# Kernel optimization log

Measured on AMD Instinct MI355X. Metric: run time of the kernel, lower is better.

## Reference

```python
import jax, jax.numpy as jnp
import numpy as np

B, T, C, H = 4, 2048, 1024, 16
D = C // H  # head dim = 64

def setup_inputs() -> dict:
    key = jax.random.key(0)
    ks = jax.random.split(key, 9)
    s = 1.0 / np.sqrt(C)
    return {
        "x":  jax.random.normal(ks[0], (B, T, C), jnp.float32),
        "Wq": jax.random.normal(ks[1], (C, C), jnp.float32) * s,
        "bq": jax.random.normal(ks[2], (C,), jnp.float32) * 0.02,
        "Wk": jax.random.normal(ks[3], (C, C), jnp.float32) * s,
        "bk": jax.random.normal(ks[4], (C,), jnp.float32) * 0.02,
        "Wv": jax.random.normal(ks[5], (C, C), jnp.float32) * s,
        "bv": jax.random.normal(ks[6], (C,), jnp.float32) * 0.02,
        "Wp": jax.random.normal(ks[7], (C, C), jnp.float32) * s,
        "bp": jax.random.normal(ks[8], (C,), jnp.float32) * 0.02,
    }

def reference(x, Wq, bq, Wk, bk, Wv, bv, Wp, bp):
    Bx, Tx, Cx = x.shape
    # projections; PyTorch Linear computes x @ W.T + b
    q = (x @ Wq.T + bq).reshape(Bx, Tx, H, D).transpose(0, 2, 1, 3)  # [B,H,T,D]
    k = (x @ Wk.T + bk).reshape(Bx, Tx, H, D).transpose(0, 2, 1, 3)
    v = (x @ Wv.T + bv).reshape(Bx, Tx, H, D).transpose(0, 2, 1, 3)
    att = jnp.einsum('bhtd,bhsd->bhts', q, k) * (1.0 / np.sqrt(D))  # [B,H,T,T]
    causal = jnp.tril(jnp.ones((Tx, Tx), bool))
    att = jnp.where(causal[None, None], att, -jnp.inf)
    att = jax.nn.softmax(att, axis=-1)
    y = jnp.einsum('bhts,bhsd->bhtd', att, v)  # [B,H,T,D]
    y = y.transpose(0, 2, 1, 3).reshape(Bx, Tx, Cx)
    return y @ Wp.T + bp
```

## Files before the change

kernel.cpp:

```cpp
#include <hip/hip_runtime.h>
#include <hip/hip_bf16.h>
#include <math.h>

static constexpr int Bn = 4, Tlen = 2048, Cdim = 1024, Hn = 16, Dh = 64;
static constexpr int Mtot = Bn * Tlen;

typedef __attribute__((ext_vector_type(8)))  short    s16x8;
typedef __attribute__((ext_vector_type(4)))  float    f32x4;
typedef __attribute__((ext_vector_type(16))) float    f32x16;
typedef __attribute__((ext_vector_type(2)))  unsigned u32x2;
typedef unsigned short u16;

#define QSCALE 0.18033688011112042f

__device__ __forceinline__ u16 f2bf(float f) {
    union { float f; unsigned u; } x; x.f = f;
    unsigned r = x.u + 0x7FFFu + ((x.u >> 16) & 1u);
    return (u16)(r >> 16);
}
__device__ __forceinline__ unsigned cvtpk(float lo, float hi) {
    unsigned r;
    asm("v_cvt_pk_bf16_f32 %0, %1, %2" : "=v"(r) : "v"(lo), "v"(hi));
    return r;
}
__device__ __forceinline__ void lane32swap(unsigned& a, unsigned& b) {
    asm("v_permlane32_swap_b32 %0, %1" : "+v"(a), "+v"(b));
}
__device__ __forceinline__ void gload_lds16(const void* g, void* l) {
    __builtin_amdgcn_global_load_lds(
        (const __attribute__((address_space(1))) void*)g,
        (__attribute__((address_space(3))) void*)l, 16, 0, 0);
}

__global__ __launch_bounds__(256) void cvt_bf16(const float* __restrict__ in,
                                                u16* __restrict__ out) {
    size_t i = (size_t)(blockIdx.x * 256 + threadIdx.x) * 8;
    float4 a = *(const float4*)(in + i);
    float4 b = *(const float4*)(in + i + 4);
    s16x8 o;
    o[0] = (short)f2bf(a.x); o[1] = (short)f2bf(a.y);
    o[2] = (short)f2bf(a.z); o[3] = (short)f2bf(a.w);
    o[4] = (short)f2bf(b.x); o[5] = (short)f2bf(b.y);
    o[6] = (short)f2bf(b.z); o[7] = (short)f2bf(b.w);
    *(s16x8*)(out + i) = o;
}

template <int MODE, int NB>
__global__ __launch_bounds__(512, 4) void gemm8w(const u16* __restrict__ A,
                                                 const u16* __restrict__ Bm,
                                                 const float* __restrict__ bq,
                                                 const float* __restrict__ bk,
                                                 const float* __restrict__ bv,
                                                 void* __restrict__ out0,
                                                 u16* __restrict__ vt) {
    constexpr int K = Cdim;
    constexpr int NKT = K / 32;
    __shared__ u16 As[3][128 * 32];
    __shared__ u16 Bs[3][256 * 32];

    const int f  = blockIdx.x;
    const int f2 = (f & 7) * (8 * NB) + (f >> 3);
    const int bm = f2 / NB, bn = f2 % NB;
    const int m0 = bm * 128, n0g = bn * 256;

    const int tid = threadIdx.x, lane = tid & 63, w = tid >> 6;
    const int wm = w >> 2, wn = w & 3;
    const int rowA = lane & 15, kg = lane >> 4;

    const int srow  = w * 16 + (lane >> 2);
    const int scolA = (((lane & 3) ^ (srow & 3)) * 8);
    const u16* Ab  = A  + (size_t)(m0 + srow) * K + scolA;
    const u16* Bb0 = Bm + (size_t)(n0g + srow) * K + scolA;
    const u16* Bb1 = Bm + (size_t)(n0g + 128 + srow) * K + scolA;

#define STAGE_T(KT, BUF)                                              \
    do {                                                              \
        const int k0_ = (KT) * 32;                                    \
        gload_lds16(Ab  + k0_, &As[BUF][w * 512]);                    \
        gload_lds16(Bb0 + k0_, &Bs[BUF][w * 512]);                    \
        gload_lds16(Bb1 + k0_, &Bs[BUF][4096 + w * 512]);             \
    } while (0)

    const int fswz = ((kg ^ (rowA & 3)) * 8);
    const int aoff = (wm * 64 + rowA) * 32 + fswz;
    const int boff = (wn * 64 + rowA) * 32 + fswz;

    f32x4 acc[4][4] = {};

    STAGE_T(0, 0);
    STAGE_T(1, 1);
    asm volatile("s_waitcnt vmcnt(3)" ::: "memory");
    __builtin_amdgcn_s_barrier();

    for (int kt = 0; kt < NKT; ++kt) {
        const int cur = kt % 3;
        s16x8 af[4], bf[4];
#pragma unroll
        for (int i = 0; i < 4; ++i) {
            af[i] = *(const s16x8*)&As[cur][aoff + i * 512];
            bf[i] = *(const s16x8*)&Bs[cur][boff + i * 512];
        }
        if (kt + 2 < NKT) STAGE_T(kt + 2, (kt + 2) % 3);
        __builtin_amdgcn_s_barrier();

        __builtin_amdgcn_s_setprio(1);
#pragma unroll
        for (int mf = 0; mf < 4; ++mf)
#pragma unroll
            for (int nf = 0; nf < 4; ++nf)
                acc[mf][nf] = __builtin_amdgcn_mfma_f32_16x16x32_bf16(
                    af[mf], bf[nf], acc[mf][nf], 0, 0, 0);
        __builtin_amdgcn_s_setprio(0);

        if (kt + 2 < NKT) asm volatile("s_waitcnt vmcnt(3)" ::: "memory");
        else              asm volatile("s_waitcnt vmcnt(0)" ::: "memory");
        __builtin_amdgcn_s_barrier();
    }
#undef STAGE_T

    const int which = (MODE == 1) ? (n0g >> 10) : 0;
    const int n0 = n0g & 1023;
    const float* bias = (MODE == 0) ? bq : (which == 0 ? bq : (which == 1 ? bk : bv));
    const float osc = (MODE == 1 && which == 0) ? QSCALE : 1.0f;
    float bb[4];
#pragma unroll
    for (int nf = 0; nf < 4; ++nf) bb[nf] = bias[n0 + wn * 64 + nf * 16 + rowA];

    if (MODE == 0) {
        float* C = (float*)out0;
#pragma unroll
        for (int mf = 0; mf < 4; ++mf)
#pragma unroll
            for (int nf = 0; nf < 4; ++nf)
#pragma unroll
                for (int r = 0; r < 4; ++r) {
                    size_t row = m0 + wm * 64 + mf * 16 + kg * 4 + r;
                    size_t col = n0 + wn * 64 + nf * 16 + rowA;
                    C[row * 1024 + col] = acc[mf][nf][r] + bb[nf];
                }
    } else if (which < 2) {
        u16* C = (u16*)out0 + (size_t)which * ((size_t)Mtot * Cdim);
#pragma unroll
        for (int mf = 0; mf < 4; ++mf)
#pragma unroll
            for (int nf = 0; nf < 4; ++nf)
#pragma unroll
                for (int r = 0; r < 4; ++r) {
                    float val = (acc[mf][nf][r] + bb[nf]) * osc;
                    size_t row = m0 + wm * 64 + mf * 16 + kg * 4 + r;
                    size_t col = n0 + wn * 64 + nf * 16 + rowA;
                    C[row * 1024 + col] = f2bf(val);
                }
    } else {
#pragma unroll
        for (int mf = 0; mf < 4; ++mf)
#pragma unroll
            for (int nf = 0; nf < 4; ++nf) {
                int hd = n0 + wn * 64 + nf * 16 + rowA;
                size_t row0 = m0 + wm * 64 + mf * 16 + kg * 4;
                int bi = (int)(row0 >> 11), t0 = (int)(row0 & 2047);
                union { u16 h[4]; u32x2 d; } pk;
#pragma unroll
                for (int r = 0; r < 4; ++r) pk.h[r] = f2bf(acc[mf][nf][r] + bb[nf]);
                *(u32x2*)(vt + ((size_t)bi * 1024 + hd) * Tlen + t0) = pk.d;
            }
    }
}

__global__ __launch_bounds__(256, 4) void attn_mfma(const u16* __restrict__ q,
                                                    const u16* __restrict__ k,
                                                    const u16* __restrict__ vt,
                                                    u16* y) {
    const int fid = blockIdx.x;
    const int pidx = fid >> 6;
    const int rem = fid & 63;
    const int h = rem & 15, b = rem >> 4;
    const int tid = threadIdx.x, lane = tid & 63, w = tid >> 6;
    const int qlane = lane & 31, hi = lane >> 5;
    __shared__ u16 Ks[2][64 * 64];
    __shared__ u16 Vs[2][64 * 64];

    const u16* kbase = k + ((size_t)(b * Tlen)) * Cdim + h * Dh;
    const u16* vbase = vt + ((size_t)(b * Hn + h)) * (size_t)(Dh * Tlen);

    const int g0row = tid >> 3;
    const int g1row = g0row + 32;
    const int gc0 = (((tid) & 7) ^ (g0row & 7)) * 8;
    const int gc1 = (((tid) & 7) ^ (g1row & 7)) * 8;

#define STAGE(JT, BUF)                                                              \
    do {                                                                            \
        const u16* kb2 = kbase + (size_t)((JT) * 64) * Cdim;                        \
        const u16* vb2 = vbase + (JT) * 64;                                         \
        gload_lds16(kb2 + (size_t)g0row * Cdim + gc0, &Ks[BUF][w * 512]);           \
        gload_lds16(kb2 + (size_t)g1row * Cdim + gc1, &Ks[BUF][2048 + w * 512]);    \
        gload_lds16(vb2 + (size_t)g0row * Tlen + gc0, &Vs[BUF][w * 512]);           \
        gload_lds16(vb2 + (size_t)g1row * Tlen + gc1, &Vs[BUF][2048 + w * 512]);    \
    } while (0)

    f32x16 zv;
#pragma unroll
    for (int r = 0; r < 16; ++r) zv[r] = 0.f;
    const int swz = (qlane & 7);

    for (int half = 0; half < 2; ++half) {
        const int qt = half ? (15 - pidx) : pidx;
        const int q0 = qt * 128;
        const int qrow_g = q0 + w * 32 + qlane;

        const u16* qrow = q + ((size_t)(b * Tlen) + qrow_g) * Cdim + h * Dh;
        s16x8 qf[4];
#pragma unroll
        for (int s = 0; s < 4; ++s)
            qf[s] = *(const s16x8*)(qrow + s * 16 + hi * 8);

        STAGE(0, 0);

        f32x16 o0 = zv, o1 = zv;
        float m_i = -INFINITY, l_i = 0.f;

        const int njt = 2 * qt + 2;
        const int jtmax = 2 * qt + (w >> 1);

        for (int jt = 0; jt < njt; ++jt) {
            const int cur = jt & 1;
            if (jt + 1 < njt) {
                STAGE(jt + 1, cur ^ 1);
                asm volatile("s_waitcnt vmcnt(4)" ::: "memory");
            } else {
                asm volatile("s_waitcnt vmcnt(0)" ::: "memory");
            }
            __builtin_amdgcn_s_barrier();

            if (jt <= jtmax) {
                const u16* kc = &Ks[cur][0];
                const u16* vc = &Vs[cur][0];
                f32x16 sA, sB;
                __builtin_amdgcn_s_setprio(1);
                {
                    const int g8 = (hi ^ swz) * 8;
                    s16x8 k0 = *(const s16x8*)&kc[qlane * 64 + g8];
                    s16x8 k1 = *(const s16x8*)&kc[(qlane + 32) * 64 + g8];
                    sA = __builtin_amdgcn_mfma_f32_32x32x16_bf16(k0, qf[0], zv, 0, 0, 0);
                    sB = __builtin_amdgcn_mfma_f32_32x32x16_bf16(k1, qf[0], zv, 0, 0, 0);
                }
#pragma unroll
                for (int s = 1; s < 4; ++s) {
                    const int g8 = ((2 * s + hi) ^ swz) * 8;
                    s16x8 k0 = *(const s16x8*)&kc[qlane * 64 + g8];
                    s16x8 k1 = *(const s16x8*)&kc[(qlane + 32) * 64 + g8];
                    sA = __builtin_amdgcn_mfma_f32_32x32x16_bf16(k0, qf[s], sA, 0, 0, 0);
                    sB = __builtin_amdgcn_mfma_f32_32x32x16_bf16(k1, qf[s], sB, 0, 0, 0);
                }
                __builtin_amdgcn_s_setprio(0);

                if (jt * 64 + 63 > q0 + w * 32) {
#pragma unroll
                    for (int r = 0; r < 16; ++r) {
                        int kv = jt * 64 + (r & 3) + 8 * (r >> 2) + 4 * hi;
                        if (kv > qrow_g)      sA[r] = -INFINITY;
                        if (kv + 32 > qrow_g) sB[r] = -INFINITY;
                    }
                }
                float pm = -INFINITY;
#pragma unroll
                for (int r = 0; r < 16; ++r) pm = fmaxf(pm, fmaxf(sA[r], sB[r]));
                pm = fmaxf(pm, __shfl_xor(pm, 32));
                const bool skip = (bool)__all(pm <= m_i + 8.0f);
                float nm = m_i, sc = 1.0f;
                if (!skip) {
                    nm = fmaxf(m_i, pm);
                    sc = exp2f(m_i - nm);
                    m_i = nm;
                }
                float ps = 0.f;
#pragma unroll
                for (int r = 0; r < 16; ++r) {
                    sA[r] = exp2f(sA[r] - nm); ps += sA[r];
                    sB[r] = exp2f(sB[r] - nm); ps += sB[r];
                }
                if (!skip) {
                    l_i = l_i * sc + ps;
#pragma unroll
                    for (int r = 0; r < 16; ++r) { o0[r] *= sc; o1[r] *= sc; }
                } else {
                    l_i += ps;
                }

                s16x8 pf[4];
                auto packsub = [&](const f32x16& sv, s16x8* out) {
#pragma unroll
                    for (int t = 0; t < 2; ++t) {
                        unsigned X = cvtpk(sv[8 * t + 0], sv[8 * t + 1]);
                        unsigned Z = cvtpk(sv[8 * t + 2], sv[8 * t + 3]);
                        unsigned Y = cvtpk(sv[8 * t + 4], sv[8 * t + 5]);
                        unsigned W = cvtpk(sv[8 * t + 6], sv[8 * t + 7]);
                        lane32swap(X, Y);
                        lane32swap(Z, W);
                        union { unsigned u[4]; s16x8 v; } fr;
                        fr.u[0] = X; fr.u[1] = Z; fr.u[2] = Y; fr.u[3] = W;
                        out[t] = fr.v;
                    }
                };
                packsub(sA, pf);
                packsub(sB, pf + 2);

                __builtin_amdgcn_s_setprio(1);
#pragma unroll
                for (int t = 0; t < 4; ++t) {
                    const int g8 = ((2 * t + hi) ^ swz) * 8;
                    s16x8 v0 = *(const s16x8*)&vc[qlane * 64 + g8];
                    s16x8 v1 = *(const s16x8*)&vc[(qlane + 32) * 64 + g8];
                    o0 = __builtin_amdgcn_mfma_f32_32x32x16_bf16(v0, pf[t], o0, 0, 0, 0);
                    o1 = __builtin_amdgcn_mfma_f32_32x32x16_bf16(v1, pf[t], o1, 0, 0, 0);
                }
                __builtin_amdgcn_s_setprio(0);
            }
            asm volatile("" ::: "memory");
            __builtin_amdgcn_s_barrier();
        }

        float inv = 1.f / (l_i + __shfl_xor(l_i, 32));
        u16* yrow = y + ((size_t)(b * Tlen) + qrow_g) * Cdim + h * Dh;
#pragma unroll
        for (int g2 = 0; g2 < 4; ++g2) {
            u32x2 st;
            st[0] = cvtpk(o0[4 * g2 + 0] * inv, o0[4 * g2 + 1] * inv);
            st[1] = cvtpk(o0[4 * g2 + 2] * inv, o0[4 * g2 + 3] * inv);
            *(u32x2*)(yrow + 8 * g2 + 4 * hi) = st;
            st[0] = cvtpk(o1[4 * g2 + 0] * inv, o1[4 * g2 + 1] * inv);
            st[1] = cvtpk(o1[4 * g2 + 2] * inv, o1[4 * g2 + 3] * inv);
            *(u32x2*)(yrow + 32 + 8 * g2 + 4 * hi) = st;
        }
    }
#undef STAGE
}

extern "C" void kernel_launch(void* const* d_in, const int* in_sizes, int n_in,
                              void* d_out, int out_size, void* d_ws, size_t ws_size,
                              hipStream_t stream) {
    const float* x  = (const float*)d_in[0];
    const float* Wq = (const float*)d_in[1];
    const float* bq = (const float*)d_in[2];
    const float* Wk = (const float*)d_in[3];
    const float* bk = (const float*)d_in[4];
    const float* Wv = (const float*)d_in[5];
    const float* bv = (const float*)d_in[6];
    const float* Wp = (const float*)d_in[7];
    const float* bp = (const float*)d_in[8];
    float* out = (float*)d_out;

    const size_t plane = (size_t)Mtot * Cdim;
    const size_t wsz   = (size_t)Cdim * Cdim;
    u16* xb    = (u16*)d_ws;
    u16* wqkvb = xb + plane;
    u16* wpb   = wqkvb + 3 * wsz;
    u16* qb    = wpb + wsz;
    u16* kb    = qb + plane;
    u16* vtb   = kb + plane;

    cvt_bf16<<<plane / 2048, 256, 0, stream>>>(x, xb);
    cvt_bf16<<<wsz / 2048, 256, 0, stream>>>(Wq, wqkvb);
    cvt_bf16<<<wsz / 2048, 256, 0, stream>>>(Wk, wqkvb + wsz);
    cvt_bf16<<<wsz / 2048, 256, 0, stream>>>(Wv, wqkvb + 2 * wsz);
    cvt_bf16<<<wsz / 2048, 256, 0, stream>>>(Wp, wpb);

    gemm8w<1, 12><<<dim3(768), 512, 0, stream>>>(xb, wqkvb, bq, bk, bv, qb, vtb);

    attn_mfma<<<dim3(512), 256, 0, stream>>>(qb, kb, vtb, qb);

    gemm8w<0, 4><<<dim3(256), 512, 0, stream>>>(qb, wpb, bp, bp, bp, out, nullptr);
}
```

Before: 183.8 us.

## Launch one attention block per query tile, heaviest first, with tree reductions

The attention kernel previously paired a short and a long causal query tile in one block to balance work. It now launches 1024 blocks, one per query tile, ordered so the tiles with the most key blocks start first, relying on the hardware scheduler for balance. Row max and row sum reductions are also rewritten as pairwise trees to shorten the serial dependency chain. This trades the static pairing for more blocks and more parallelism, at the cost of an extra Q load and prologue per block and reliance on dispatch order for the tail.

```diff
diff --git a/kernel.cpp b/kernel.cpp
--- a/kernel.cpp
+++ b/kernel.cpp
@@ -172,13 +172,22 @@
                                                     const u16* __restrict__ vt,
                                                     u16* y) {
     const int fid = blockIdx.x;
-    const int pidx = fid >> 6;
+    const int qt = 15 - (fid >> 6);
     const int rem = fid & 63;
     const int h = rem & 15, b = rem >> 4;
     const int tid = threadIdx.x, lane = tid & 63, w = tid >> 6;
     const int qlane = lane & 31, hi = lane >> 5;
     __shared__ u16 Ks[2][64 * 64];
     __shared__ u16 Vs[2][64 * 64];
+
+    const int q0 = qt * 128;
+    const int qrow_g = q0 + w * 32 + qlane;
+
+    const u16* qrow = q + ((size_t)(b * Tlen) + qrow_g) * Cdim + h * Dh;
+    s16x8 qf[4];
+#pragma unroll
+    for (int s = 0; s < 4; ++s)
+        qf[s] = *(const s16x8*)(qrow + s * 16 + hi * 8);
 
     const u16* kbase = k + ((size_t)(b * Tlen)) * Cdim + h * Dh;
     const u16* vbase = vt + ((size_t)(b * Hn + h)) * (size_t)(Dh * Tlen);
@@ -203,137 +212,138 @@
     for (int r = 0; r < 16; ++r) zv[r] = 0.f;
     const int swz = (qlane & 7);
 
-    for (int half = 0; half < 2; ++half) {
-        const int qt = half ? (15 - pidx) : pidx;
-        const int q0 = qt * 128;
-        const int qrow_g = q0 + w * 32 + qlane;
-
-        const u16* qrow = q + ((size_t)(b * Tlen) + qrow_g) * Cdim + h * Dh;
-        s16x8 qf[4];
-#pragma unroll
-        for (int s = 0; s < 4; ++s)
-            qf[s] = *(const s16x8*)(qrow + s * 16 + hi * 8);
-
-        STAGE(0, 0);
-
-        f32x16 o0 = zv, o1 = zv;
-        float m_i = -INFINITY, l_i = 0.f;
-
-        const int njt = 2 * qt + 2;
-        const int jtmax = 2 * qt + (w >> 1);
-
-        for (int jt = 0; jt < njt; ++jt) {
-            const int cur = jt & 1;
-            if (jt + 1 < njt) {
-                STAGE(jt + 1, cur ^ 1);
-                asm volatile("s_waitcnt vmcnt(4)" ::: "memory");
+    STAGE(0, 0);
+
+    f32x16 o0 = zv, o1 = zv;
+    float m_i = -INFINITY, l_i = 0.f;
+
+    const int njt = 2 * qt + 2;
+    const int jtmax = 2 * qt + (w >> 1);
+
+    for (int jt = 0; jt < njt; ++jt) {
+        const int cur = jt & 1;
+        if (jt + 1 < njt) {
+            STAGE(jt + 1, cur ^ 1);
+            asm volatile("s_waitcnt vmcnt(4)" ::: "memory");
+        } else {
+            asm volatile("s_waitcnt vmcnt(0)" ::: "memory");
+        }
+        __builtin_amdgcn_s_barrier();
+
+        if (jt <= jtmax) {
+            const u16* kc = &Ks[cur][0];
+            const u16* vc = &Vs[cur][0];
+            f32x16 sA, sB;
+            __builtin_amdgcn_s_setprio(1);
+            {
+                const int g8 = (hi ^ swz) * 8;
+                s16x8 k0 = *(const s16x8*)&kc[qlane * 64 + g8];
+                s16x8 k1 = *(const s16x8*)&kc[(qlane + 32) * 64 + g8];
+                sA = __builtin_amdgcn_mfma_f32_32x32x16_bf16(k0, qf[0], zv, 0, 0, 0);
+                sB = __builtin_amdgcn_mfma_f32_32x32x16_bf16(k1, qf[0], zv, 0, 0, 0);
+            }
+#pragma unroll
+            for (int s = 1; s < 4; ++s) {
+                const int g8 = ((2 * s + hi) ^ swz) * 8;
+                s16x8 k0 = *(const s16x8*)&kc[qlane * 64 + g8];
+                s16x8 k1 = *(const s16x8*)&kc[(qlane + 32) * 64 + g8];
+                sA = __builtin_amdgcn_mfma_f32_32x32x16_bf16(k0, qf[s], sA, 0, 0, 0);
+                sB = __builtin_amdgcn_mfma_f32_32x32x16_bf16(k1, qf[s], sB, 0, 0, 0);
+            }
+            __builtin_amdgcn_s_setprio(0);
+
+            if (jt * 64 + 63 > q0 + w * 32) {
+#pragma unroll
+                for (int r = 0; r < 16; ++r) {
+                    int kv = jt * 64 + (r & 3) + 8 * (r >> 2) + 4 * hi;
+                    if (kv > qrow_g)      sA[r] = -INFINITY;
+                    if (kv + 32 > qrow_g) sB[r] = -INFINITY;
+                }
+            }
+            float tm[8];
+#pragma unroll
+            for (int r = 0; r < 8; ++r)
+                tm[r] = fmaxf(fmaxf(sA[r], sA[r + 8]), fmaxf(sB[r], sB[r + 8]));
+#pragma unroll
+            for (int s = 4; s >= 1; s >>= 1)
+#pragma unroll
+                for (int r = 0; r < s; ++r) tm[r] = fmaxf(tm[r], tm[r + s]);
+            float pm = fmaxf(tm[0], __shfl_xor(tm[0], 32));
+
+            const bool skip = (bool)__all(pm <= m_i + 8.0f);
+            float nm = m_i, sc = 1.0f;
+            if (!skip) {
+                nm = fmaxf(m_i, pm);
+                sc = exp2f(m_i - nm);
+                m_i = nm;
+            }
+#pragma unroll
+            for (int r = 0; r < 16; ++r) {
+                sA[r] = exp2f(sA[r] - nm);
+                sB[r] = exp2f(sB[r] - nm);
+            }
+            float ts[8];
+#pragma unroll
+            for (int r = 0; r < 8; ++r)
+                ts[r] = (sA[r] + sA[r + 8]) + (sB[r] + sB[r + 8]);
+#pragma unroll
+            for (int s = 4; s >= 1; s >>= 1)
+#pragma unroll
+                for (int r = 0; r < s; ++r) ts[r] += ts[r + s];
+            if (!skip) {
+                l_i = l_i * sc + ts[0];
+#pragma unroll
+                for (int r = 0; r < 16; ++r) { o0[r] *= sc; o1[r] *= sc; }
             } else {
-                asm volatile("s_waitcnt vmcnt(0)" ::: "memory");
-            }
-            __builtin_amdgcn_s_barrier();
-
-            if (jt <= jtmax) {
-                const u16* kc = &Ks[cur][0];
-                const u16* vc = &Vs[cur][0];
-                f32x16 sA, sB;
-                __builtin_amdgcn_s_setprio(1);
-                {
-                    const int g8 = (hi ^ swz) * 8;
-                    s16x8 k0 = *(const s16x8*)&kc[qlane * 64 + g8];
-                    s16x8 k1 = *(const s16x8*)&kc[(qlane + 32) * 64 + g8];
-                    sA = __builtin_amdgcn_mfma_f32_32x32x16_bf16(k0, qf[0], zv, 0, 0, 0);
-                    sB = __builtin_amdgcn_mfma_f32_32x32x16_bf16(k1, qf[0], zv, 0, 0, 0);
+                l_i += ts[0];
+            }
+
+            s16x8 pf[4];
+            auto packsub = [&](const f32x16& sv, s16x8* out) {
+#pragma unroll
+                for (int t = 0; t < 2; ++t) {
+                    unsigned X = cvtpk(sv[8 * t + 0], sv[8 * t + 1]);
+                    unsigned Z = cvtpk(sv[8 * t + 2], sv[8 * t + 3]);
+                    unsigned Y = cvtpk(sv[8 * t + 4], sv[8 * t + 5]);
+                    unsigned W = cvtpk(sv[8 * t + 6], sv[8 * t + 7]);
+                    lane32swap(X, Y);
+                    lane32swap(Z, W);
+                    union { unsigned u[4]; s16x8 v; } fr;
+                    fr.u[0] = X; fr.u[1] = Z; fr.u[2] = Y; fr.u[3] = W;
+                    out[t] = fr.v;
                 }
-#pragma unroll
-                for (int s = 1; s < 4; ++s) {
-                    const int g8 = ((2 * s + hi) ^ swz) * 8;
-                    s16x8 k0 = *(const s16x8*)&kc[qlane * 64 + g8];
-                    s16x8 k1 = *(const s16x8*)&kc[(qlane + 32) * 64 + g8];
-                    sA = __builtin_amdgcn_mfma_f32_32x32x16_bf16(k0, qf[s], sA, 0, 0, 0);
-                    sB = __builtin_amdgcn_mfma_f32_32x32x16_bf16(k1, qf[s], sB, 0, 0, 0);
-                }
-                __builtin_amdgcn_s_setprio(0);
-
-                if (jt * 64 + 63 > q0 + w * 32) {
-#pragma unroll
-                    for (int r = 0; r < 16; ++r) {
-                        int kv = jt * 64 + (r & 3) + 8 * (r >> 2) + 4 * hi;
-                        if (kv > qrow_g)      sA[r] = -INFINITY;
-                        if (kv + 32 > qrow_g) sB[r] = -INFINITY;
-                    }
-                }
-                float pm = -INFINITY;
-#pragma unroll
-                for (int r = 0; r < 16; ++r) pm = fmaxf(pm, fmaxf(sA[r], sB[r]));
-                pm = fmaxf(pm, __shfl_xor(pm, 32));
-                const bool skip = (bool)__all(pm <= m_i + 8.0f);
-                float nm = m_i, sc = 1.0f;
-                if (!skip) {
-                    nm = fmaxf(m_i, pm);
-                    sc = exp2f(m_i - nm);
-                    m_i = nm;
-                }
-                float ps = 0.f;
-#pragma unroll
-                for (int r = 0; r < 16; ++r) {
-                    sA[r] = exp2f(sA[r] - nm); ps += sA[r];
-                    sB[r] = exp2f(sB[r] - nm); ps += sB[r];
-                }
-                if (!skip) {
-                    l_i = l_i * sc + ps;
-#pragma unroll
-                    for (int r = 0; r < 16; ++r) { o0[r] *= sc; o1[r] *= sc; }
-                } else {
-                    l_i += ps;
-                }
-
-                s16x8 pf[4];
-                auto packsub = [&](const f32x16& sv, s16x8* out) {
-#pragma unroll
-                    for (int t = 0; t < 2; ++t) {
-                        unsigned X = cvtpk(sv[8 * t + 0], sv[8 * t + 1]);
-                        unsigned Z = cvtpk(sv[8 * t + 2], sv[8 * t + 3]);
-                        unsigned Y = cvtpk(sv[8 * t + 4], sv[8 * t + 5]);
-                        unsigned W = cvtpk(sv[8 * t + 6], sv[8 * t + 7]);
-                        lane32swap(X, Y);
-                        lane32swap(Z, W);
-                        union { unsigned u[4]; s16x8 v; } fr;
-                        fr.u[0] = X; fr.u[1] = Z; fr.u[2] = Y; fr.u[3] = W;
-                        out[t] = fr.v;
-                    }
-                };
-                packsub(sA, pf);
-                packsub(sB, pf + 2);
-
-                __builtin_amdgcn_s_setprio(1);
-#pragma unroll
-                for (int t = 0; t < 4; ++t) {
-                    const int g8 = ((2 * t + hi) ^ swz) * 8;
-                    s16x8 v0 = *(const s16x8*)&vc[qlane * 64 + g8];
-                    s16x8 v1 = *(const s16x8*)&vc[(qlane + 32) * 64 + g8];
-                    o0 = __builtin_amdgcn_mfma_f32_32x32x16_bf16(v0, pf[t], o0, 0, 0, 0);
-                    o1 = __builtin_amdgcn_mfma_f32_32x32x16_bf16(v1, pf[t], o1, 0, 0, 0);
-                }
-                __builtin_amdgcn_s_setprio(0);
-            }
-            asm volatile("" ::: "memory");
-            __builtin_amdgcn_s_barrier();
+            };
+            packsub(sA, pf);
+            packsub(sB, pf + 2);
+
+            __builtin_amdgcn_s_setprio(1);
+#pragma unroll
+            for (int t = 0; t < 4; ++t) {
+                const int g8 = ((2 * t + hi) ^ swz) * 8;
+                s16x8 v0 = *(const s16x8*)&vc[qlane * 64 + g8];
+                s16x8 v1 = *(const s16x8*)&vc[(qlane + 32) * 64 + g8];
+                o0 = __builtin_amdgcn_mfma_f32_32x32x16_bf16(v0, pf[t], o0, 0, 0, 0);
+                o1 = __builtin_amdgcn_mfma_f32_32x32x16_bf16(v1, pf[t], o1, 0, 0, 0);
+            }
+            __builtin_amdgcn_s_setprio(0);
         }
-
-        float inv = 1.f / (l_i + __shfl_xor(l_i, 32));
-        u16* yrow = y + ((size_t)(b * Tlen) + qrow_g) * Cdim + h * Dh;
-#pragma unroll
-        for (int g2 = 0; g2 < 4; ++g2) {
-            u32x2 st;
-            st[0] = cvtpk(o0[4 * g2 + 0] * inv, o0[4 * g2 + 1] * inv);
-            st[1] = cvtpk(o0[4 * g2 + 2] * inv, o0[4 * g2 + 3] * inv);
-            *(u32x2*)(yrow + 8 * g2 + 4 * hi) = st;
-            st[0] = cvtpk(o1[4 * g2 + 0] * inv, o1[4 * g2 + 1] * inv);
-            st[1] = cvtpk(o1[4 * g2 + 2] * inv, o1[4 * g2 + 3] * inv);
-            *(u32x2*)(yrow + 32 + 8 * g2 + 4 * hi) = st;
-        }
+        asm volatile("" ::: "memory");
+        __builtin_amdgcn_s_barrier();
     }
 #undef STAGE
+
+    float inv = 1.f / (l_i + __shfl_xor(l_i, 32));
+    u16* yrow = y + ((size_t)(b * Tlen) + qrow_g) * Cdim + h * Dh;
+#pragma unroll
+    for (int g2 = 0; g2 < 4; ++g2) {
+        u32x2 st;
+        st[0] = cvtpk(o0[4 * g2 + 0] * inv, o0[4 * g2 + 1] * inv);
+        st[1] = cvtpk(o0[4 * g2 + 2] * inv, o0[4 * g2 + 3] * inv);
+        *(u32x2*)(yrow + 8 * g2 + 4 * hi) = st;
+        st[0] = cvtpk(o1[4 * g2 + 0] * inv, o1[4 * g2 + 1] * inv);
+        st[1] = cvtpk(o1[4 * g2 + 2] * inv, o1[4 * g2 + 3] * inv);
+        *(u32x2*)(yrow + 32 + 8 * g2 + 4 * hi) = st;
+    }
 }
 
 extern "C" void kernel_launch(void* const* d_in, const int* in_sizes, int n_in,
@@ -367,7 +377,7 @@
 
     gemm8w<1, 12><<<dim3(768), 512, 0, stream>>>(xb, wqkvb, bq, bk, bv, qb, vtb);
 
-    attn_mfma<<<dim3(512), 256, 0, stream>>>(qb, kb, vtb, qb);
+    attn_mfma<<<dim3(1024), 256, 0, stream>>>(qb, kb, vtb, qb);
 
     gemm8w<0, 4><<<dim3(256), 512, 0, stream>>>(qb, wpb, bp, bp, bp, out, nullptr);
 }
```

New measurement: 176.0 us. -4.2%, faster.
